# Optimization experiments

Hardware: AMD Instinct MI355X
Metric: run time of the kernel (lower is better)

The kernel has to match this reference:

```python
import jax, jax.numpy as jnp
import numpy as np

B, N, D, H = 4, 2048, 1024, 8
HD = D // H  # head_dim = 128
TEMPER = 1.0
LN_EPS = 1e-5


def setup_inputs() -> dict:
    key = jax.random.key(0)
    ks = jax.random.split(key, 6)
    return {
        "h": jax.random.normal(ks[0], (B, N, D), dtype=jnp.float32),
        "Wl": jax.random.normal(ks[1], (D, D), dtype=jnp.float32) * (D ** -0.5),
        "Wr": jax.random.normal(ks[2], (D, D), dtype=jnp.float32) * (D ** -0.5),
        "att_l": jax.random.normal(ks[3], (1, HD), dtype=jnp.float32) * (HD ** -0.5),
        "att_r": jax.random.normal(ks[4], (1, HD), dtype=jnp.float32) * (HD ** -0.5),
        "Wf": jax.random.normal(ks[5], (D, D), dtype=jnp.float32) * (D ** -0.5),
        "ln_gamma": jnp.ones((D,), dtype=jnp.float32),
        "ln_beta": jnp.zeros((D,), dtype=jnp.float32),
    }


def _leaky(x):
    return jnp.where(x > 0, x, 0.01 * x)


def reference(h, Wl, Wr, att_l, att_r, Wf, ln_gamma, ln_beta):
    b, n, d = h.shape
    # projections -> [B, H, N, HD]
    fl = (h @ Wl.T).reshape(b, n, H, HD).transpose(0, 2, 1, 3)
    fr = (h @ Wr.T).reshape(b, n, H, HD).transpose(0, 2, 1, 3)
    # additive (GAT-style) scores: sl[b,h,i] + sr[b,h,j]
    sl = jnp.einsum("bhnd,d->bhn", _leaky(fl), att_l[0])
    sr = jnp.einsum("bhnd,d->bhn", _leaky(fr), att_r[0])
    score = (sl[:, :, :, None] + sr[:, :, None, :]) / TEMPER  # [B,H,N,N]
    p = jax.nn.softmax(score, axis=-1)
    # context and merge heads
    ctx = jnp.einsum("bhnm,bhmd->bhnd", p, fr)
    h_sa = ctx.transpose(0, 2, 1, 3).reshape(b, n, d)
    fh = h_sa @ Wf.T
    y = h + fh
    mu = jnp.mean(y, axis=-1, keepdims=True)
    var = jnp.mean(jnp.square(y - mu), axis=-1, keepdims=True)
    return (y - mu) * jax.lax.rsqrt(var + LN_EPS) * ln_gamma + ln_beta
```

## Files before the change

kernel.cpp:

```cpp
#include <hip/hip_runtime.h>
#include <hip/hip_bf16.h>

#define B_ 4
#define N_ 2048
#define D_ 1024
#define H_ 8
#define HD_ 128

typedef __attribute__((ext_vector_type(4))) float f32x4;
typedef __attribute__((ext_vector_type(8))) short bf16x8;

__device__ __forceinline__ short f2bf(float f) {
    unsigned u = __builtin_bit_cast(unsigned, f);
    u = (u + 0x7FFFu + ((u >> 16) & 1u)) >> 16;
    return (short)u;
}
__device__ __forceinline__ float bf2f(unsigned short s) {
    unsigned u = (unsigned)s << 16;
    return __builtin_bit_cast(float, u);
}

typedef const __attribute__((address_space(1))) void* gas_t;
typedef __attribute__((address_space(3))) void* las_t;

__device__ __forceinline__ void gload16(const void* g, void* l) {
    __builtin_amdgcn_global_load_lds((gas_t)g, (las_t)l, 16, 0, 0);
}

__global__ __launch_bounds__(256) void k_cvt(
    const float* __restrict__ h, short* __restrict__ hb,
    const float* __restrict__ Wr, short* __restrict__ wrb)
{
    int blk = blockIdx.x;
    const float* src;
    short* dst;
    int i;
    if (blk < 4096) { src = h;  dst = hb;  i = blk * 256 + threadIdx.x; }
    else            { src = Wr; dst = wrb; i = (blk - 4096) * 256 + threadIdx.x; }
    float4 a = ((const float4*)src)[i * 2];
    float4 b = ((const float4*)src)[i * 2 + 1];
    bf16x8 o;
    o[0] = f2bf(a.x); o[1] = f2bf(a.y); o[2] = f2bf(a.z); o[3] = f2bf(a.w);
    o[4] = f2bf(b.x); o[5] = f2bf(b.y); o[6] = f2bf(b.z); o[7] = f2bf(b.w);
    ((bf16x8*)dst)[i] = o;
}

__global__ __launch_bounds__(256) void k_proj_sr(
    const short* __restrict__ hb, const short* __restrict__ wrb,
    const float* __restrict__ att_r, float* __restrict__ sr)
{
    __shared__ short sA[128 * 32];
    __shared__ short sB[128 * 32];
    __shared__ float part[2][128];

    const int tid  = threadIdx.x;
    const int lane = tid & 63;
    const int wave = tid >> 6;
    const int cc   = lane & 15;
    const int g    = lane >> 4;
    const int wr   = wave >> 1;
    const int wc   = wave & 1;
    const int rowBase = blockIdx.x * 128;
    const int head    = blockIdx.y;

    const int r0q0 = (wave * 2) * 16 + (lane >> 2);
    const int colb = (lane & 3) * 8;
    const short* gA0 = hb  + (size_t)(rowBase + r0q0) * D_ + colb;
    const short* gB0 = wrb + (size_t)(head * HD_ + r0q0) * D_ + colb;
    char* lA = (char*)sA + (size_t)(wave * 2) * 1024;
    char* lB = (char*)sB + (size_t)(wave * 2) * 1024;

    f32x4 acc[4][4];
#pragma unroll
    for (int m = 0; m < 4; ++m)
#pragma unroll
        for (int n = 0; n < 4; ++n) acc[m][n] = (f32x4){0.f, 0.f, 0.f, 0.f};

    for (int k0 = 0; k0 < D_; k0 += 32) {
        gload16(gA0 + k0,            lA);
        gload16(gA0 + k0 + 16 * D_,  lA + 1024);
        gload16(gB0 + k0,            lB);
        gload16(gB0 + k0 + 16 * D_,  lB + 1024);
        __syncthreads();

        bf16x8 aF[4], bF[4];
#pragma unroll
        for (int m = 0; m < 4; ++m)
            aF[m] = *(const bf16x8*)(sA + ((wr * 64 + m * 16 + cc) * 32 + g * 8));
#pragma unroll
        for (int n = 0; n < 4; ++n)
            bF[n] = *(const bf16x8*)(sB + ((wc * 64 + n * 16 + cc) * 32 + g * 8));
#pragma unroll
        for (int m = 0; m < 4; ++m)
#pragma unroll
            for (int n = 0; n < 4; ++n)
                acc[m][n] = __builtin_amdgcn_mfma_f32_16x16x32_bf16(
                    aF[m], bF[n], acc[m][n], 0, 0, 0);
        __syncthreads();
    }

    float ar[4];
#pragma unroll
    for (int n = 0; n < 4; ++n) ar[n] = att_r[wc * 64 + n * 16 + cc];

#pragma unroll
    for (int m = 0; m < 4; ++m) {
#pragma unroll
        for (int r = 0; r < 4; ++r) {
            float p = 0.f;
#pragma unroll
            for (int n = 0; n < 4; ++n) {
                float v = acc[m][n][r];
                v = v > 0.f ? v : 0.01f * v;
                p += v * ar[n];
            }
            p += __shfl_xor(p, 1); p += __shfl_xor(p, 2);
            p += __shfl_xor(p, 4); p += __shfl_xor(p, 8);
            if (cc == 0) part[wc][wr * 64 + m * 16 + g * 4 + r] = p;
        }
    }
    __syncthreads();
    if (tid < 128) {
        const int grow = rowBase + tid;
        const int b = grow >> 11, j = grow & (N_ - 1);
        sr[(size_t)(b * H_ + head) * N_ + j] = part[0][tid] + part[1][tid];
    }
}

__global__ __launch_bounds__(256) void k_hbar(
    const short* __restrict__ hbm, const float* __restrict__ sr,
    float* __restrict__ hp)
{
    const int dc = blockIdx.x;
    const int jc = blockIdx.y;
    const int b  = blockIdx.z;
    const int tid = threadIdx.x;
    const int d = dc * 256 + tid;

    __shared__ float smx[8], sism[8];
    {
        const int hh = tid >> 5;
        const int sl = tid & 31;
        const float4* row = (const float4*)(sr + (size_t)(b * H_ + hh) * N_);
        float4 v[16];
        float mx = -1e30f;
#pragma unroll
        for (int k = 0; k < 16; ++k) {
            v[k] = row[sl + k * 32];
            mx = fmaxf(fmaxf(mx, fmaxf(v[k].x, v[k].y)), fmaxf(v[k].z, v[k].w));
        }
#pragma unroll
        for (int m = 1; m < 32; m <<= 1) mx = fmaxf(mx, __shfl_xor(mx, m));
        float sum = 0.f;
#pragma unroll
        for (int k = 0; k < 16; ++k)
            sum += expf(v[k].x - mx) + expf(v[k].y - mx) +
                   expf(v[k].z - mx) + expf(v[k].w - mx);
#pragma unroll
        for (int m = 1; m < 32; m <<= 1) sum += __shfl_xor(sum, m);
        if (sl == 0) { smx[hh] = mx; sism[hh] = 1.f / sum; }
    }
    __syncthreads();

    __shared__ float wl[8][128];
    for (int idx = tid; idx < 1024; idx += 256) {
        const int hh = idx >> 7, jj = idx & 127;
        wl[hh][jj] = expf(sr[(size_t)(b * H_ + hh) * N_ + jc * 128 + jj]
                          - smx[hh]) * sism[hh];
    }
    __syncthreads();

    float acc[8] = {0.f, 0.f, 0.f, 0.f, 0.f, 0.f, 0.f, 0.f};
    const short* hp0 = hbm + ((size_t)(b * N_ + jc * 128)) * D_ + d;
#pragma unroll 4
    for (int jj = 0; jj < 128; ++jj) {
        float hv = bf2f((unsigned short)hp0[(size_t)jj * D_]);
#pragma unroll
        for (int hh = 0; hh < 8; ++hh) acc[hh] += wl[hh][jj] * hv;
    }
#pragma unroll
    for (int hh = 0; hh < 8; ++hh)
        hp[((size_t)(jc * 32) + b * 8 + hh) * D_ + d] = acc[hh];
}

__global__ __launch_bounds__(256) void k_ctx(
    const float* __restrict__ hp, const float* __restrict__ Wr,
    float* __restrict__ ctx)
{
    const int bh = blockIdx.x >> 5;
    const int b = bh >> 3, head = bh & 7;
    const int dg = (blockIdx.x & 31) * 4;
    const int tid = threadIdx.x;
    const int lane = tid & 63, wave = tid >> 6;

    __shared__ float xs[1024];
    float4 s = {0.f, 0.f, 0.f, 0.f};
#pragma unroll
    for (int jc = 0; jc < 16; ++jc) {
        float4 v = ((const float4*)(hp + ((size_t)(jc * 32) + bh) * D_))[tid];
        s.x += v.x; s.y += v.y; s.z += v.z; s.w += v.w;
    }
    ((float4*)xs)[tid] = s;
    __syncthreads();

    const int o = dg + wave;
    const float* wrow = Wr + (size_t)(head * HD_ + o) * D_;
    float acc = 0.f;
#pragma unroll
    for (int it = 0; it < 4; ++it) {
        float4 wv = *(const float4*)(wrow + it * 256 + lane * 4);
        float4 xv = ((const float4*)xs)[it * 64 + lane];
        acc += wv.x * xv.x + wv.y * xv.y + wv.z * xv.z + wv.w * xv.w;
    }
#pragma unroll
    for (int m = 1; m < 64; m <<= 1) acc += __shfl_xor(acc, m);
    if (lane == 0) ctx[(size_t)b * D_ + head * HD_ + o] = acc;
}

__global__ __launch_bounds__(256) void k_fvec(
    const float* __restrict__ ctx, const float* __restrict__ Wf,
    float* __restrict__ fvec)
{
    const int o = blockIdx.x * 4 + (threadIdx.x >> 6);
    const int lane = threadIdx.x & 63;
    const int b = o >> 10, orow = o & 1023;
    const float* x  = ctx + (size_t)b * D_;
    const float* wf = Wf + (size_t)orow * D_;
    float s = 0.f;
#pragma unroll
    for (int it = 0; it < 4; ++it) {
        float4 xv = *(const float4*)(x + it * 256 + lane * 4);
        float4 wv = *(const float4*)(wf + it * 256 + lane * 4);
        s += xv.x * wv.x + xv.y * wv.y + xv.z * wv.z + xv.w * wv.w;
    }
#pragma unroll
    for (int m = 1; m < 64; m <<= 1) s += __shfl_xor(s, m);
    if (lane == 0) fvec[o] = s;
}

__global__ __launch_bounds__(256) void k_ln(
    const short* __restrict__ hbm, const float* __restrict__ fvec,
    const float* __restrict__ gamma, const float* __restrict__ beta,
    float* __restrict__ out)
{
    const int row = blockIdx.x;
    const int b = row >> 11;
    const int tid = threadIdx.x;
    const int lane = tid & 63, wave = tid >> 6;

    short4 hv4 = *(const short4*)(hbm + (size_t)row * D_ + tid * 4);
    float4 fv = *(const float4*)(fvec + (size_t)b * D_ + tid * 4);
    const float y0 = bf2f((unsigned short)hv4.x) + fv.x;
    const float y1 = bf2f((unsigned short)hv4.y) + fv.y;
    const float y2 = bf2f((unsigned short)hv4.z) + fv.z;
    const float y3 = bf2f((unsigned short)hv4.w) + fv.w;

    float s = y0 + y1 + y2 + y3;
    float q = y0 * y0 + y1 * y1 + y2 * y2 + y3 * y3;
#pragma unroll
    for (int m = 1; m < 64; m <<= 1) { s += __shfl_xor(s, m); q += __shfl_xor(q, m); }

    __shared__ float rs[4], rq[4];
    if (lane == 0) { rs[wave] = s; rq[wave] = q; }
    __syncthreads();
    s = rs[0] + rs[1] + rs[2] + rs[3];
    q = rq[0] + rq[1] + rq[2] + rq[3];

    const float mu  = s * (1.f / D_);
    const float var = q * (1.f / D_) - mu * mu;
    const float inv = rsqrtf(var + 1e-5f);

    float4 gv = *(const float4*)(gamma + tid * 4);
    float4 bv = *(const float4*)(beta + tid * 4);
    float4 ov;
    ov.x = (y0 - mu) * inv * gv.x + bv.x;
    ov.y = (y1 - mu) * inv * gv.y + bv.y;
    ov.z = (y2 - mu) * inv * gv.z + bv.z;
    ov.w = (y3 - mu) * inv * gv.w + bv.w;
    *(float4*)(out + (size_t)row * D_ + tid * 4) = ov;
}

extern "C" void kernel_launch(void* const* d_in, const int* in_sizes, int n_in,
                              void* d_out, int out_size, void* d_ws, size_t ws_size,
                              hipStream_t stream) {
    const float* h     = (const float*)d_in[0];
    const float* Wr    = (const float*)d_in[2];
    const float* att_r = (const float*)d_in[4];
    const float* Wf    = (const float*)d_in[5];
    const float* gamma = (const float*)d_in[6];
    const float* beta  = (const float*)d_in[7];
    float* out = (float*)d_out;

    char* ws = (char*)d_ws;
    float* sr    = (float*)(ws);
    float* hp    = (float*)(ws + 524288);
    float* ctx   = (float*)(ws + 2752512);
    float* fvec  = (float*)(ws + 2768896);
    short* hb    = (short*)(ws + 4194304);
    short* wrb   = (short*)(ws + 4194304 + 16777216);

    k_cvt<<<4096 + 512, 256, 0, stream>>>(h, hb, Wr, wrb);
    k_proj_sr<<<dim3(B_ * N_ / 128, H_), 256, 0, stream>>>(hb, wrb, att_r, sr);
    k_hbar<<<dim3(4, 16, 4), 256, 0, stream>>>(hb, sr, hp);
    k_ctx<<<1024, 256, 0, stream>>>(hp, Wr, ctx);
    k_fvec<<<1024, 256, 0, stream>>>(ctx, Wf, fvec);
    k_ln<<<B_ * N_, 256, 0, stream>>>(hb, fvec, gamma, beta, out);
}
```

Baseline: 73.99 us.

## Double K-tile depth to 64 with XOR-swizzled LDS layout in sr projection

The sr projection GEMM now stages a 64-wide K slice per iteration instead of 32, which halves the number of barrier pairs and loop iterations. The LDS tiles use 128-byte rows with an XOR swizzle on the 16-byte column chunk, applied both to the global-to-LDS load address and to the fragment reads, to avoid bank conflicts. This doubles LDS use per block and could reduce occupancy.

```diff
diff --git a/kernel.cpp b/kernel.cpp
--- a/kernel.cpp
+++ b/kernel.cpp
@@ -49,8 +49,8 @@
     const short* __restrict__ hb, const short* __restrict__ wrb,
     const float* __restrict__ att_r, float* __restrict__ sr)
 {
-    __shared__ short sA[128 * 32];
-    __shared__ short sB[128 * 32];
+    __shared__ short sA[128 * 64];
+    __shared__ short sB[128 * 64];
     __shared__ float part[2][128];
 
     const int tid  = threadIdx.x;
@@ -63,12 +63,12 @@
     const int rowBase = blockIdx.x * 128;
     const int head    = blockIdx.y;
 
-    const int r0q0 = (wave * 2) * 16 + (lane >> 2);
-    const int colb = (lane & 3) * 8;
-    const short* gA0 = hb  + (size_t)(rowBase + r0q0) * D_ + colb;
-    const short* gB0 = wrb + (size_t)(head * HD_ + r0q0) * D_ + colb;
-    char* lA = (char*)sA + (size_t)(wave * 2) * 1024;
-    char* lB = (char*)sB + (size_t)(wave * 2) * 1024;
+    const int srow = lane >> 3;
+    const int scol = ((lane & 7) ^ srow) * 8;
+    const short* gA0 = hb  + (size_t)(rowBase + wave * 32 + srow) * D_ + scol;
+    const short* gB0 = wrb + (size_t)(head * HD_ + wave * 32 + srow) * D_ + scol;
+    char* lA = (char*)sA + wave * 32 * 128;
+    char* lB = (char*)sB + wave * 32 * 128;
 
     f32x4 acc[4][4];
 #pragma unroll
@@ -76,26 +76,36 @@
 #pragma unroll
         for (int n = 0; n < 4; ++n) acc[m][n] = (f32x4){0.f, 0.f, 0.f, 0.f};
 
-    for (int k0 = 0; k0 < D_; k0 += 32) {
-        gload16(gA0 + k0,            lA);
-        gload16(gA0 + k0 + 16 * D_,  lA + 1024);
-        gload16(gB0 + k0,            lB);
-        gload16(gB0 + k0 + 16 * D_,  lB + 1024);
+    for (int k0 = 0; k0 < D_; k0 += 64) {
+#pragma unroll
+        for (int q = 0; q < 4; ++q) {
+            gload16(gA0 + k0 + q * 8 * D_, lA + q * 1024);
+            gload16(gB0 + k0 + q * 8 * D_, lB + q * 1024);
+        }
         __syncthreads();
 
-        bf16x8 aF[4], bF[4];
-#pragma unroll
-        for (int m = 0; m < 4; ++m)
-            aF[m] = *(const bf16x8*)(sA + ((wr * 64 + m * 16 + cc) * 32 + g * 8));
-#pragma unroll
-        for (int n = 0; n < 4; ++n)
-            bF[n] = *(const bf16x8*)(sB + ((wc * 64 + n * 16 + cc) * 32 + g * 8));
-#pragma unroll
-        for (int m = 0; m < 4; ++m)
-#pragma unroll
-            for (int n = 0; n < 4; ++n)
-                acc[m][n] = __builtin_amdgcn_mfma_f32_16x16x32_bf16(
-                    aF[m], bF[n], acc[m][n], 0, 0, 0);
+#pragma unroll
+        for (int kk = 0; kk < 2; ++kk) {
+            bf16x8 aF[4], bF[4];
+#pragma unroll
+            for (int m = 0; m < 4; ++m) {
+                const int row = wr * 64 + m * 16 + cc;
+                const int ks  = (kk * 64 + g * 16) ^ ((cc & 7) << 4);
+                aF[m] = *(const bf16x8*)((const char*)sA + row * 128 + ks);
+            }
+#pragma unroll
+            for (int n = 0; n < 4; ++n) {
+                const int row = wc * 64 + n * 16 + cc;
+                const int ks  = (kk * 64 + g * 16) ^ ((cc & 7) << 4);
+                bF[n] = *(const bf16x8*)((const char*)sB + row * 128 + ks);
+            }
+#pragma unroll
+            for (int m = 0; m < 4; ++m)
+#pragma unroll
+                for (int n = 0; n < 4; ++n)
+                    acc[m][n] = __builtin_amdgcn_mfma_f32_16x16x32_bf16(
+                        aF[m], bF[n], acc[m][n], 0, 0, 0);
+        }
         __syncthreads();
     }
 
```

Result: faster. 69.71 us (-5.8%).
